# Optimization experiments

Measured on AMD Instinct MI355X. Metric: run time of the kernel, lower is better.

## Reference

```python
import jax, jax.numpy as jnp
import numpy as np

N_NODES = 4_000_000
N_GRAPHS = 4096  # B; fixed for jit (torch derives it from batch.max()+1)
D_FEAT = 8
NUM_CLASSES = 10


def setup_inputs() -> dict:
    key = jax.random.key(0)
    k1, k2, k3, k4, k5 = jax.random.split(key, 5)
    x = jax.random.normal(k1, (N_NODES, D_FEAT), dtype=jnp.float32)
    # sorted segment ids; with ~977 nodes/graph expected, empty segments are vanishingly unlikely
    batch_ids = jnp.sort(jax.random.randint(k2, (N_NODES,), 0, N_GRAPHS, dtype=jnp.int64))
    input_ids = jax.random.randint(k3, (N_GRAPHS, 128), 0, 30522, dtype=jnp.int64)
    attention_mask = jnp.ones((N_GRAPHS, 128), dtype=jnp.int64)
    W = jax.random.normal(k4, (NUM_CLASSES, D_FEAT), dtype=jnp.float32) * (1.0 / np.sqrt(D_FEAT))
    b = jax.random.normal(k5, (NUM_CLASSES,), dtype=jnp.float32) * 0.01
    return {"x": x, "batch_ids": batch_ids, "input_ids": input_ids,
            "attention_mask": attention_mask, "W": W, "b": b}


def reference(x, batch_ids, input_ids, attention_mask, W, b):
    # Segment-mean pooling: replaces the O(B) python loop of masked means
    # with a single-pass scatter-add. input_ids / attention_mask are unused
    # by the original forward (kept for signature fidelity).
    sums = jax.ops.segment_sum(x, batch_ids, num_segments=N_GRAPHS)          # [B, 8]
    counts = jax.ops.segment_sum(jnp.ones((x.shape[0],), x.dtype), batch_ids,
                                 num_segments=N_GRAPHS)                      # [B]
    pooled = sums / counts[:, None]                                          # [B, 8]
    logits = pooled @ W.T + b                                                # [B, 10]
    return logits
```

## Files before the change

kernel.cpp:

```cpp
#include <hip/hip_runtime.h>

constexpr int N_NODES  = 4000000;
constexpr int N_GRAPHS = 4096;
constexpr int D_FEAT   = 8;
constexpr int N_CLS    = 10;
constexpr int CHUNK    = 512;
constexpr int NCH      = (N_NODES + CHUNK - 1) / CHUNK;
constexpr int ACC_F32  = N_GRAPHS * D_FEAT + N_GRAPHS;
constexpr int ZBLK     = ACC_F32 / (256 * 4);

static_assert(ACC_F32 % (256 * 4) == 0, "zero region must tile exactly");

typedef float f32x4 __attribute__((ext_vector_type(4)));
typedef int   i32x4 __attribute__((ext_vector_type(4)));


__global__ __launch_bounds__(256) void scan_zero(
    const i32x4* __restrict__ ids4, const int* __restrict__ ids,
    int* __restrict__ bounds, float* __restrict__ acc)
{
    if (blockIdx.x < ZBLK) {
        int z = (blockIdx.x * 256 + threadIdx.x) * 4;
        *(f32x4*)(acc + z) = (f32x4)(0.f);
    }

    int t = blockIdx.x * blockDim.x + threadIdx.x;
    int base = t * 4;
    if (base >= N_NODES) return;

    i32x4 v = ids4[t];
    int prev = (base == 0) ? -1 : ids[base - 1];

    int cur;
    cur = v.x; if (cur != prev) { for (int g = prev + 1; g <= cur; ++g) bounds[g] = base + 0; } prev = cur;
    cur = v.y; if (cur != prev) { for (int g = prev + 1; g <= cur; ++g) bounds[g] = base + 1; } prev = cur;
    cur = v.z; if (cur != prev) { for (int g = prev + 1; g <= cur; ++g) bounds[g] = base + 2; } prev = cur;
    cur = v.w; if (cur != prev) { for (int g = prev + 1; g <= cur; ++g) bounds[g] = base + 3; } prev = cur;

    if (base + 4 >= N_NODES) {
        for (int g = prev + 1; g <= N_GRAPHS; ++g) bounds[g] = N_NODES;
    }
}

__global__ __launch_bounds__(256, 8) void pool_atomic(
    const f32x4* __restrict__ xf,
    const int*   __restrict__ ids,
    const int*   __restrict__ bounds,
    float*       __restrict__ sums,
    float*       __restrict__ cnts)
{
    int w = blockIdx.x * 4 + (threadIdx.x >> 6);
    if (w >= NCH) return;
    int lane = threadIdx.x & 63;

    int c0 = w * CHUNK;
    int c1 = min(c0 + CHUNK, N_NODES);
    int g0 = ids[c0];
    int g1 = ids[c1 - 1];

    int p = c0, gcur = g0;
    while (true) {
        int pend = (gcur < g1) ? bounds[gcur + 1] : c1;
        f32x4 a0 = (f32x4)(0.f), a1 = (f32x4)(0.f),
              a2 = (f32x4)(0.f), a3 = (f32x4)(0.f);
        int i = 2 * p + lane;
        int endf = 2 * pend;
        int full = (endf - 2 * p) >> 8;
        for (int it = 0; it < full; ++it, i += 256) {
            a0 += xf[i];
            a1 += xf[i +  64];
            a2 += xf[i + 128];
            a3 += xf[i + 192];
        }
        for (; i < endf; i += 64) a0 += xf[i];
        f32x4 acc = (a0 + a1) + (a2 + a3);

        #pragma unroll
        for (int off = 32; off >= 2; off >>= 1) {
            acc.x += __shfl_xor(acc.x, off);
            acc.y += __shfl_xor(acc.y, off);
            acc.z += __shfl_xor(acc.z, off);
            acc.w += __shfl_xor(acc.w, off);
        }
        if (lane < 2 && pend > p) {
            float* s = sums + (size_t)gcur * D_FEAT + lane * 4;
            atomicAdd(s + 0, acc.x);
            atomicAdd(s + 1, acc.y);
            atomicAdd(s + 2, acc.z);
            atomicAdd(s + 3, acc.w);
        }
        if (lane == 0 && pend > p)
            atomicAdd(cnts + gcur, (float)(pend - p));

        if (pend >= c1) break;
        p = pend;
        ++gcur;
    }
}

__global__ __launch_bounds__(256) void finalize(
    const float* __restrict__ sums, const float* __restrict__ cnts,
    const float* __restrict__ W, const float* __restrict__ bias,
    float* __restrict__ out)
{
    int idx = blockIdx.x * blockDim.x + threadIdx.x;
    if (idx >= N_GRAPHS * N_CLS) return;
    int g = idx / N_CLS;
    int c = idx % N_CLS;
    float inv = 1.0f / cnts[g];
    const float* s = sums + (size_t)g * D_FEAT;
    const float* w = W + (size_t)c * D_FEAT;
    float a = bias[c];
    #pragma unroll
    for (int k = 0; k < D_FEAT; ++k)
        a += (s[k] * inv) * w[k];
    out[idx] = a;
}

extern "C" void kernel_launch(void* const* d_in, const int* in_sizes, int n_in,
                              void* d_out, int out_size, void* d_ws, size_t ws_size,
                              hipStream_t stream) {
    const float* x   = (const float*)d_in[0];
    const int*   ids = (const int*)d_in[1];
    const float* W   = (const float*)d_in[4];
    const float* b   = (const float*)d_in[5];
    float*       out = (float*)d_out;

    float* sums   = (float*)d_ws;
    float* cnts   = sums + (size_t)N_GRAPHS * D_FEAT;
    int*   bounds = (int*)(cnts + N_GRAPHS);

    int scan_blocks = (N_NODES / 4 + 255) / 256;
    scan_zero<<<scan_blocks, 256, 0, stream>>>(
        (const i32x4*)ids, ids, bounds, sums);

    int pool_blocks = (NCH + 3) / 4;
    pool_atomic<<<pool_blocks, 256, 0, stream>>>(
        (const f32x4*)x, ids, bounds, sums, cnts);

    finalize<<<(N_GRAPHS * N_CLS + 255) / 256, 256, 0, stream>>>(
        sums, cnts, W, b, out);
}
```

Before: 33.16 us.

## Fuse segment-boundary detection into pooling kernel via per-warp ballot

Drops the separate scan kernel that wrote a global bounds array. Each wavefront now loads the segment ids for its 512-node chunk in registers and finds the next segment change with a ballot and shuffle, then reduces x over that run. Zeroing the accumulators moves to hipMemsetAsync. This removes one full pass over the 16 MB id array and the dependent bounds lookups, at the cost of extra ballot/shuffle work per segment inside the pooling loop.

```diff
diff --git a/kernel.cpp b/kernel.cpp
--- a/kernel.cpp
+++ b/kernel.cpp
@@ -7,63 +7,65 @@
 constexpr int CHUNK    = 512;
 constexpr int NCH      = (N_NODES + CHUNK - 1) / CHUNK;
 constexpr int ACC_F32  = N_GRAPHS * D_FEAT + N_GRAPHS;
-constexpr int ZBLK     = ACC_F32 / (256 * 4);
-
-static_assert(ACC_F32 % (256 * 4) == 0, "zero region must tile exactly");
 
 typedef float f32x4 __attribute__((ext_vector_type(4)));
 typedef int   i32x4 __attribute__((ext_vector_type(4)));
 
 
-__global__ __launch_bounds__(256) void scan_zero(
-    const i32x4* __restrict__ ids4, const int* __restrict__ ids,
-    int* __restrict__ bounds, float* __restrict__ acc)
-{
-    if (blockIdx.x < ZBLK) {
-        int z = (blockIdx.x * 256 + threadIdx.x) * 4;
-        *(f32x4*)(acc + z) = (f32x4)(0.f);
-    }
-
-    int t = blockIdx.x * blockDim.x + threadIdx.x;
-    int base = t * 4;
-    if (base >= N_NODES) return;
-
-    i32x4 v = ids4[t];
-    int prev = (base == 0) ? -1 : ids[base - 1];
-
-    int cur;
-    cur = v.x; if (cur != prev) { for (int g = prev + 1; g <= cur; ++g) bounds[g] = base + 0; } prev = cur;
-    cur = v.y; if (cur != prev) { for (int g = prev + 1; g <= cur; ++g) bounds[g] = base + 1; } prev = cur;
-    cur = v.z; if (cur != prev) { for (int g = prev + 1; g <= cur; ++g) bounds[g] = base + 2; } prev = cur;
-    cur = v.w; if (cur != prev) { for (int g = prev + 1; g <= cur; ++g) bounds[g] = base + 3; } prev = cur;
-
-    if (base + 4 >= N_NODES) {
-        for (int g = prev + 1; g <= N_GRAPHS; ++g) bounds[g] = N_NODES;
-    }
-}
-
-__global__ __launch_bounds__(256, 8) void pool_atomic(
+__global__ __launch_bounds__(256) void pool_seg(
     const f32x4* __restrict__ xf,
+    const i32x4* __restrict__ ids4,
     const int*   __restrict__ ids,
-    const int*   __restrict__ bounds,
     float*       __restrict__ sums,
     float*       __restrict__ cnts)
 {
     int w = blockIdx.x * 4 + (threadIdx.x >> 6);
     if (w >= NCH) return;
     int lane = threadIdx.x & 63;
-
     int c0 = w * CHUNK;
     int c1 = min(c0 + CHUNK, N_NODES);
-    int g0 = ids[c0];
-    int g1 = ids[c1 - 1];
 
-    int p = c0, gcur = g0;
+    int base = c0 + lane * 8;
+    i32x4 v0, v1;
+    if (base + 8 <= N_NODES) {
+        v0 = ids4[base >> 2];
+        v1 = ids4[(base >> 2) + 1];
+    } else {
+        int last = ids[N_NODES - 1];
+        v0 = (i32x4)(last);
+        v1 = (i32x4)(last);
+    }
+    int gcur = __shfl(v0.x, 0);
+    int p = c0;
+
     while (true) {
-        int pend = (gcur < g1) ? bounds[gcur + 1] : c1;
+        unsigned m8 = 0;
+        m8 |= (v0.x != gcur && base + 0 > p) ? 1u   : 0u;
+        m8 |= (v0.y != gcur && base + 1 > p) ? 2u   : 0u;
+        m8 |= (v0.z != gcur && base + 2 > p) ? 4u   : 0u;
+        m8 |= (v0.w != gcur && base + 3 > p) ? 8u   : 0u;
+        m8 |= (v1.x != gcur && base + 4 > p) ? 16u  : 0u;
+        m8 |= (v1.y != gcur && base + 5 > p) ? 32u  : 0u;
+        m8 |= (v1.z != gcur && base + 6 > p) ? 64u  : 0u;
+        m8 |= (v1.w != gcur && base + 7 > p) ? 128u : 0u;
+
+        int j0   = __builtin_ctz(m8 | 0x100u);
+        int cpos = base + j0;
+        int cid  = j0 < 4 ? (j0 < 2 ? (j0 == 0 ? v0.x : v0.y)
+                                    : (j0 == 2 ? v0.z : v0.w))
+                          : (j0 < 6 ? (j0 == 4 ? v1.x : v1.y)
+                                    : (j0 == 6 ? v1.z : v1.w));
+        unsigned long long ball = __ballot(m8 != 0);
+        int pend = c1, gnext = 0;
+        if (ball != 0ull) {
+            int fl = __builtin_ctzll(ball);
+            pend  = __shfl(cpos, fl);
+            gnext = __shfl(cid,  fl);
+        }
+
         f32x4 a0 = (f32x4)(0.f), a1 = (f32x4)(0.f),
               a2 = (f32x4)(0.f), a3 = (f32x4)(0.f);
-        int i = 2 * p + lane;
+        int i    = 2 * p + lane;
         int endf = 2 * pend;
         int full = (endf - 2 * p) >> 8;
         for (int it = 0; it < full; ++it, i += 256) {
@@ -82,19 +84,18 @@
             acc.z += __shfl_xor(acc.z, off);
             acc.w += __shfl_xor(acc.w, off);
         }
-        if (lane < 2 && pend > p) {
+        if (lane < 2) {
             float* s = sums + (size_t)gcur * D_FEAT + lane * 4;
             atomicAdd(s + 0, acc.x);
             atomicAdd(s + 1, acc.y);
             atomicAdd(s + 2, acc.z);
             atomicAdd(s + 3, acc.w);
         }
-        if (lane == 0 && pend > p)
+        if (lane == 0)
             atomicAdd(cnts + gcur, (float)(pend - p));
 
         if (pend >= c1) break;
-        p = pend;
-        ++gcur;
+        p = pend; gcur = gnext;
     }
 }
 
@@ -126,17 +127,14 @@
     const float* b   = (const float*)d_in[5];
     float*       out = (float*)d_out;
 
-    float* sums   = (float*)d_ws;
-    float* cnts   = sums + (size_t)N_GRAPHS * D_FEAT;
-    int*   bounds = (int*)(cnts + N_GRAPHS);
+    float* sums = (float*)d_ws;
+    float* cnts = sums + (size_t)N_GRAPHS * D_FEAT;
 
-    int scan_blocks = (N_NODES / 4 + 255) / 256;
-    scan_zero<<<scan_blocks, 256, 0, stream>>>(
-        (const i32x4*)ids, ids, bounds, sums);
+    hipMemsetAsync(d_ws, 0, (size_t)ACC_F32 * sizeof(float), stream);
 
     int pool_blocks = (NCH + 3) / 4;
-    pool_atomic<<<pool_blocks, 256, 0, stream>>>(
-        (const f32x4*)x, ids, bounds, sums, cnts);
+    pool_seg<<<pool_blocks, 256, 0, stream>>>(
+        (const f32x4*)x, (const i32x4*)ids, ids, sums, cnts);
 
     finalize<<<(N_GRAPHS * N_CLS + 255) / 256, 256, 0, stream>>>(
         sums, cnts, W, b, out);
```

After: 35.47 us. +7.0%, slower.
